# Kernel optimization log

Hardware: AMD Instinct MI355X
Metric: run time of the kernel (lower is better)

Reference implementation:

```python
import jax, jax.numpy as jnp
import numpy as np

K = 7  # window_size


def setup_inputs() -> dict:
    key = jax.random.key(0)
    ks = jax.random.split(key, 6)
    B, S, C, H, W = 2, 5, 256, 192, 192
    hidden = max(C // 16, 4)  # 16
    return {
        "x": jax.random.normal(ks[0], (B, S, C, H, W), dtype=jnp.float32),
        "w1": jax.random.normal(ks[1], (hidden, C), dtype=jnp.float32) * 0.05,
        "b1": jax.random.normal(ks[2], (hidden,), dtype=jnp.float32) * 0.05,
        "w2": jax.random.normal(ks[3], (1, hidden), dtype=jnp.float32) * 0.05,
        "b2": jax.random.normal(ks[4], (1,), dtype=jnp.float32) * 0.05,
        "static_logits": jax.random.normal(ks[5], (5,), dtype=jnp.float32) * 0.05,
    }


def reference(x, w1, b1, w2, b2, static_logits):
    # x: [B, S, C, H, W]
    B, S, C, H, W = x.shape
    k = K
    pad_h = (k - H % k) % k
    pad_w = (k - W % k) % k
    xp = jnp.pad(x, ((0, 0), (0, 0), (0, 0), (0, pad_h), (0, pad_w)))
    Hp, Wp = H + pad_h, W + pad_w
    nH, nW = Hp // k, Wp // k
    # replicate torch unfold(3,k,k).unfold(4,k,k) -> [B,S,C,nH,nW,k,k]
    xw = xp.reshape(B, S, C, nH, k, nW, k).transpose(0, 1, 2, 3, 5, 4, 6)
    # window means: [B,S,C,nH,nW]
    g = xw.mean(axis=(-1, -2))
    # permute to [B,nH,nW,S,C] and apply tiny MLP over C
    gp = g.transpose(0, 3, 4, 1, 2)
    h = jax.nn.relu(jnp.einsum('bnmsc,hc->bnmsh', gp, w1) + b1)
    logits = jnp.einsum('bnmsh,oh->bnmso', h, w2)[..., 0] + b2[0]
    logits = logits + static_logits  # broadcast over S (last axis)
    wts = jax.nn.softmax(logits, axis=-1)       # [B,nH,nW,S]
    wt = wts.transpose(0, 3, 1, 2)              # [B,S,nH,nW]
    # softmax-weighted sum over slices: [B,C,nH,nW,kH,kW]
    fused = jnp.einsum('bscnmhw,bsnm->bcnmhw', xw, wt)
    # faithful to torch: permute(0,1,4,2,5,3) then reshape (note: this is the
    # exact layout the original code produces, even though it interleaves
    # window and grid axes differently from the unfold inverse)
    out = fused.transpose(0, 1, 4, 2, 5, 3).reshape(B, C, Hp, Wp)
    return out[:, :, :H, :W]
```

## Files before the change

### kernel.cpp

```cpp
#include <hip/hip_runtime.h>

#define B_ 2
#define S_ 5
#define C_ 256
#define H_ 192
#define W_ 192
#define K_ 7
#define NH_ 28
#define NW_ 28
#define HID_ 16


__global__ void k_means(const float* __restrict__ x, float* __restrict__ g) {
    int idx = blockIdx.x;
    int n = idx % NH_; idx /= NH_;
    int c = idx % C_;  idx /= C_;
    int s = idx % S_;  idx /= S_;
    int b = idx;
    const float* plane = x + ((size_t)((b * S_ + s) * C_ + c)) * (H_ * W_);
    __shared__ float colsum[W_];
    int j = threadIdx.x;
    float acc = 0.f;
    int r0 = n * K_;
#pragma unroll
    for (int kh = 0; kh < K_; ++kh) {
        int r = r0 + kh;
        if (r < H_) acc += plane[r * W_ + j];
    }
    colsum[j] = acc;
    __syncthreads();
    if (j < NW_) {
        float ssum = 0.f;
        int c0 = j * K_;
#pragma unroll
        for (int d = 0; d < K_; ++d) {
            int cc = c0 + d;
            if (cc < W_) ssum += colsum[cc];
        }
        g[((size_t)((b * NH_ + n) * NW_ + j)) * (S_ * C_) + s * C_ + c] =
            ssum * (1.0f / 49.0f);
    }
}

__global__ void k_mlp(const float* __restrict__ g, const float* __restrict__ w1,
                      const float* __restrict__ b1, const float* __restrict__ w2,
                      const float* __restrict__ b2, const float* __restrict__ sl,
                      float* __restrict__ wt) {
    int site = blockIdx.x;
    int m = site % NW_;
    int n = (site / NW_) % NH_;
    int b = site / (NW_ * NH_);
    int s = threadIdx.x >> 6;
    int lane = threadIdx.x & 63;
    const float* gv = g + (size_t)site * (S_ * C_) + s * C_;
    float x0 = gv[lane];
    float x1 = gv[lane + 64];
    float x2 = gv[lane + 128];
    float x3 = gv[lane + 192];
    float logit = 0.f;
#pragma unroll
    for (int jj = 0; jj < HID_; ++jj) {
        const float* wr = w1 + jj * C_;
        float p = wr[lane] * x0 + wr[lane + 64] * x1 +
                  wr[lane + 128] * x2 + wr[lane + 192] * x3;
#pragma unroll
        for (int o = 1; o < 64; o <<= 1) p += __shfl_xor(p, o, 64);
        float h = p + b1[jj];
        h = h > 0.f ? h : 0.f;
        logit = fmaf(w2[jj], h, logit);
    }
    __shared__ float lg[S_];
    if (lane == 0) lg[s] = logit + b2[0] + sl[s];
    __syncthreads();
    if (threadIdx.x < S_) {
        int ss = threadIdx.x;
        float mx = lg[0];
#pragma unroll
        for (int t = 1; t < S_; ++t) mx = fmaxf(mx, lg[t]);
        float den = 0.f;
#pragma unroll
        for (int t = 0; t < S_; ++t) den += expf(lg[t] - mx);
        wt[((b * S_ + ss) * NH_ + n) * NW_ + m] = expf(lg[ss] - mx) / den;
    }
}

__global__ void k_out(const float* __restrict__ x, const float* __restrict__ wt,
                      float* __restrict__ out) {
    int idx = blockIdx.x;
    int i = idx % H_; idx /= H_;
    int c = idx % C_; idx /= C_;
    int b = idx;
    int n = i % NH_, kh = i / NH_;
    int r = n * K_ + kh;
    int j = threadIdx.x;
    size_t obase = (((size_t)(b * C_ + c)) * H_ + i) * (size_t)W_;
    if (r >= H_) {
        out[obase + j] = 0.f;
        return;
    }
    __shared__ float srow[S_][W_];
    __shared__ float wrow[S_][NW_];
#pragma unroll
    for (int s = 0; s < S_; ++s) {
        srow[s][j] = x[(((size_t)((b * S_ + s) * C_ + c)) * H_ + r) * W_ + j];
    }
    if (j < S_ * NW_) {
        int s = j / NW_, mm = j % NW_;
        wrow[s][mm] = wt[((b * S_ + s) * NH_ + n) * NW_ + mm];
    }
    __syncthreads();
    int m = j % NW_, kw = j / NW_;
    int col = m * K_ + kw;
    float val = 0.f;
#pragma unroll
    for (int s = 0; s < S_; ++s) {
        float v = (col < W_) ? srow[s][col] : 0.f;
        val = fmaf(wrow[s][m], v, val);
    }
    out[obase + j] = val;
}

extern "C" void kernel_launch(void* const* d_in, const int* in_sizes, int n_in,
                              void* d_out, int out_size, void* d_ws, size_t ws_size,
                              hipStream_t stream) {
    const float* x  = (const float*)d_in[0];
    const float* w1 = (const float*)d_in[1];
    const float* b1 = (const float*)d_in[2];
    const float* w2 = (const float*)d_in[3];
    const float* b2 = (const float*)d_in[4];
    const float* sl = (const float*)d_in[5];
    float* out = (float*)d_out;

    float* g  = (float*)d_ws;
    float* wt = g + (size_t)B_ * NH_ * NW_ * S_ * C_;

    k_means<<<B_ * S_ * C_ * NH_, 192, 0, stream>>>(x, g);
    k_mlp<<<B_ * NH_ * NW_, 5 * 64, 0, stream>>>(g, w1, b1, w2, b2, sl, wt);
    k_out<<<B_ * C_ * H_, 192, 0, stream>>>(x, wt, out);
}
```

Before: 611.9 us.

## Restructure all three kernels with float4 loads and per-plane/window-row blocking

The means kernel now processes a whole plane per block with float4 loads, four waves each covering window rows, and writes g in [b,s,c,site] layout. The MLP kernel assigns one site per lane and loops over channels with per-thread hidden accumulators, replacing the wave-wide shuffle reductions but launching only 26 blocks. The output kernel loads a full 7-row band for all slices into shared memory with float4 and writes all output rows that map to that band. The aim is fewer blocks, wider coalesced loads and less launch overhead, at the cost of a very small MLP grid and more shared memory per block.

```diff
diff --git a/kernel.cpp b/kernel.cpp
--- a/kernel.cpp
+++ b/kernel.cpp
@@ -8,116 +8,141 @@
 #define K_ 7
 #define NH_ 28
 #define NW_ 28
+#define NSITE_ 784
 #define HID_ 16
 
 
-__global__ void k_means(const float* __restrict__ x, float* __restrict__ g) {
+__global__ __launch_bounds__(256) void k_means(const float* __restrict__ x,
+                                               float* __restrict__ g) {
+    int idx = blockIdx.x;
+    const float* plane = x + (size_t)idx * (H_ * W_);
+    float* gout = g + (size_t)idx * NSITE_;
+    __shared__ float colsum[4][W_];
+    int w = threadIdx.x >> 6;
+    int lane = threadIdx.x & 63;
+    for (int t = w; t < NH_; t += 4) {
+        if (lane < 48) {
+            const float* rp = plane + (7 * t) * W_ + 4 * lane;
+            float4 cs = make_float4(0.f, 0.f, 0.f, 0.f);
+            if (7 * t + 7 <= H_) {
+#pragma unroll
+                for (int r = 0; r < 7; ++r) {
+                    float4 v = *(const float4*)(rp + r * W_);
+                    cs.x += v.x; cs.y += v.y; cs.z += v.z; cs.w += v.w;
+                }
+            } else {
+#pragma unroll
+                for (int r = 0; r < 3; ++r) {
+                    float4 v = *(const float4*)(rp + r * W_);
+                    cs.x += v.x; cs.y += v.y; cs.z += v.z; cs.w += v.w;
+                }
+            }
+            *(float4*)&colsum[w][4 * lane] = cs;
+        }
+        __syncthreads();
+        if (lane < NW_) {
+            int c0 = lane * 7;
+            float ssum = 0.f;
+#pragma unroll
+            for (int d = 0; d < 7; ++d) {
+                int cc = c0 + d;
+                if (cc < W_) ssum += colsum[w][cc];
+            }
+            gout[t * NW_ + lane] = ssum * (1.0f / 49.0f);
+        }
+        __syncthreads();
+    }
+}
+
+__global__ __launch_bounds__(320) void k_mlp(const float* __restrict__ g,
+                                             const float* __restrict__ w1,
+                                             const float* __restrict__ b1,
+                                             const float* __restrict__ w2,
+                                             const float* __restrict__ b2,
+                                             const float* __restrict__ sl,
+                                             float* __restrict__ wt) {
+    int b = blockIdx.x / 13;
+    int chunk = blockIdx.x % 13;
+    int s = threadIdx.x >> 6;
+    int lane = threadIdx.x & 63;
+    int site = chunk * 64 + lane;
+    bool valid = site < NSITE_;
+    int site_c = valid ? site : (NSITE_ - 1);
+    const float* gp = g + ((size_t)(b * S_ + s) * C_) * NSITE_ + site_c;
+    float h[HID_];
+#pragma unroll
+    for (int j = 0; j < HID_; ++j) h[j] = 0.f;
+#pragma unroll 4
+    for (int c = 0; c < C_; ++c) {
+        float gv = gp[(size_t)c * NSITE_];
+#pragma unroll
+        for (int j = 0; j < HID_; ++j) h[j] = fmaf(w1[j * C_ + c], gv, h[j]);
+    }
+    float logit = b2[0] + sl[s];
+#pragma unroll
+    for (int j = 0; j < HID_; ++j) {
+        float hv = h[j] + b1[j];
+        hv = hv > 0.f ? hv : 0.f;
+        logit = fmaf(w2[j], hv, logit);
+    }
+    __shared__ float lg[S_][64];
+    lg[s][lane] = logit;
+    __syncthreads();
+    if (valid) {
+        float l0 = lg[0][lane], l1 = lg[1][lane], l2 = lg[2][lane],
+              l3 = lg[3][lane], l4 = lg[4][lane];
+        float mx = fmaxf(fmaxf(fmaxf(l0, l1), fmaxf(l2, l3)), l4);
+        float e0 = expf(l0 - mx), e1 = expf(l1 - mx), e2 = expf(l2 - mx),
+              e3 = expf(l3 - mx), e4 = expf(l4 - mx);
+        float inv = 1.f / (e0 + e1 + e2 + e3 + e4);
+        float es = (s == 0) ? e0 : (s == 1) ? e1 : (s == 2) ? e2
+                 : (s == 3) ? e3 : e4;
+        wt[(b * S_ + s) * NSITE_ + site] = es * inv;
+    }
+}
+
+__global__ __launch_bounds__(448) void k_out(const float* __restrict__ x,
+                                             const float* __restrict__ wt,
+                                             float* __restrict__ out) {
     int idx = blockIdx.x;
     int n = idx % NH_; idx /= NH_;
     int c = idx % C_;  idx /= C_;
-    int s = idx % S_;  idx /= S_;
     int b = idx;
-    const float* plane = x + ((size_t)((b * S_ + s) * C_ + c)) * (H_ * W_);
-    __shared__ float colsum[W_];
-    int j = threadIdx.x;
-    float acc = 0.f;
-    int r0 = n * K_;
-#pragma unroll
-    for (int kh = 0; kh < K_; ++kh) {
-        int r = r0 + kh;
-        if (r < H_) acc += plane[r * W_ + j];
+    __shared__ float srow[S_][7 * W_];
+    __shared__ float wrow[S_][NW_];
+    int tid = threadIdx.x;
+    int r0 = 7 * n;
+    int nrows = (H_ - r0 < 7) ? (H_ - r0) : 7;
+    int nf4 = nrows * (W_ / 4);
+    for (int t = tid; t < S_ * 336; t += 448) {
+        int s = t / 336, tt = t - s * 336;
+        const float4* src = (const float4*)(x +
+            (((size_t)((b * S_ + s) * C_ + c)) * H_ + r0) * W_);
+        ((float4*)&srow[s][0])[tt] =
+            (tt < nf4) ? src[tt] : make_float4(0.f, 0.f, 0.f, 0.f);
     }
-    colsum[j] = acc;
-    __syncthreads();
-    if (j < NW_) {
-        float ssum = 0.f;
-        int c0 = j * K_;
-#pragma unroll
-        for (int d = 0; d < K_; ++d) {
-            int cc = c0 + d;
-            if (cc < W_) ssum += colsum[cc];
-        }
-        g[((size_t)((b * NH_ + n) * NW_ + j)) * (S_ * C_) + s * C_ + c] =
-            ssum * (1.0f / 49.0f);
-    }
-}
-
-__global__ void k_mlp(const float* __restrict__ g, const float* __restrict__ w1,
-                      const float* __restrict__ b1, const float* __restrict__ w2,
-                      const float* __restrict__ b2, const float* __restrict__ sl,
-                      float* __restrict__ wt) {
-    int site = blockIdx.x;
-    int m = site % NW_;
-    int n = (site / NW_) % NH_;
-    int b = site / (NW_ * NH_);
-    int s = threadIdx.x >> 6;
-    int lane = threadIdx.x & 63;
-    const float* gv = g + (size_t)site * (S_ * C_) + s * C_;
-    float x0 = gv[lane];
-    float x1 = gv[lane + 64];
-    float x2 = gv[lane + 128];
-    float x3 = gv[lane + 192];
-    float logit = 0.f;
-#pragma unroll
-    for (int jj = 0; jj < HID_; ++jj) {
-        const float* wr = w1 + jj * C_;
-        float p = wr[lane] * x0 + wr[lane + 64] * x1 +
-                  wr[lane + 128] * x2 + wr[lane + 192] * x3;
-#pragma unroll
-        for (int o = 1; o < 64; o <<= 1) p += __shfl_xor(p, o, 64);
-        float h = p + b1[jj];
-        h = h > 0.f ? h : 0.f;
-        logit = fmaf(w2[jj], h, logit);
-    }
-    __shared__ float lg[S_];
-    if (lane == 0) lg[s] = logit + b2[0] + sl[s];
-    __syncthreads();
-    if (threadIdx.x < S_) {
-        int ss = threadIdx.x;
-        float mx = lg[0];
-#pragma unroll
-        for (int t = 1; t < S_; ++t) mx = fmaxf(mx, lg[t]);
-        float den = 0.f;
-#pragma unroll
-        for (int t = 0; t < S_; ++t) den += expf(lg[t] - mx);
-        wt[((b * S_ + ss) * NH_ + n) * NW_ + m] = expf(lg[ss] - mx) / den;
-    }
-}
-
-__global__ void k_out(const float* __restrict__ x, const float* __restrict__ wt,
-                      float* __restrict__ out) {
-    int idx = blockIdx.x;
-    int i = idx % H_; idx /= H_;
-    int c = idx % C_; idx /= C_;
-    int b = idx;
-    int n = i % NH_, kh = i / NH_;
-    int r = n * K_ + kh;
-    int j = threadIdx.x;
-    size_t obase = (((size_t)(b * C_ + c)) * H_ + i) * (size_t)W_;
-    if (r >= H_) {
-        out[obase + j] = 0.f;
-        return;
-    }
-    __shared__ float srow[S_][W_];
-    __shared__ float wrow[S_][NW_];
-#pragma unroll
-    for (int s = 0; s < S_; ++s) {
-        srow[s][j] = x[(((size_t)((b * S_ + s) * C_ + c)) * H_ + r) * W_ + j];
-    }
-    if (j < S_ * NW_) {
-        int s = j / NW_, mm = j % NW_;
-        wrow[s][mm] = wt[((b * S_ + s) * NH_ + n) * NW_ + mm];
+    if (tid < S_ * NW_) {
+        int s = tid / NW_, m = tid % NW_;
+        wrow[s][m] = wt[(b * S_ + s) * NSITE_ + n * NW_ + m];
     }
     __syncthreads();
-    int m = j % NW_, kw = j / NW_;
-    int col = m * K_ + kw;
-    float val = 0.f;
 #pragma unroll
-    for (int s = 0; s < S_; ++s) {
-        float v = (col < W_) ? srow[s][col] : 0.f;
-        val = fmaf(wrow[s][m], v, val);
+    for (int it = 0; it < 3; ++it) {
+        int o = it * 448 + tid;
+        int kh = o / W_, j = o - kh * W_;
+        int i = NH_ * kh + n;
+        if (i >= H_) continue;
+        int m = j % NW_, kw = j / NW_;
+        int col = m * K_ + kw;
+        float val = 0.f;
+        if (col < W_) {
+            const float* sp = &srow[0][kh * W_ + col];
+#pragma unroll
+            for (int s = 0; s < S_; ++s)
+                val = fmaf(wrow[s][m], srow[s][kh * W_ + col], val);
+        }
+        out[(((size_t)(b * C_ + c)) * H_ + i) * (size_t)W_ + j] = val;
     }
-    out[obase + j] = val;
 }
 
 extern "C" void kernel_launch(void* const* d_in, const int* in_sizes, int n_in,
@@ -132,9 +157,9 @@
     float* out = (float*)d_out;
 
     float* g  = (float*)d_ws;
-    float* wt = g + (size_t)B_ * NH_ * NW_ * S_ * C_;
+    float* wt = g + (size_t)B_ * S_ * C_ * NSITE_;
 
-    k_means<<<B_ * S_ * C_ * NH_, 192, 0, stream>>>(x, g);
-    k_mlp<<<B_ * NH_ * NW_, 5 * 64, 0, stream>>>(g, w1, b1, w2, b2, sl, wt);
-    k_out<<<B_ * C_ * H_, 192, 0, stream>>>(x, wt, out);
+    k_means<<<B_ * S_ * C_, 256, 0, stream>>>(x, g);
+    k_mlp<<<B_ * 13, 320, 0, stream>>>(g, w1, b1, w2, b2, sl, wt);
+    k_out<<<B_ * C_ * NH_, 448, 0, stream>>>(x, wt, out);
 }
```

New measurement: 645.0 us. 1.05x slower.
